# Kernel tuning notes

Hardware: AMD Instinct MI355X
Metric: run time of the kernel (lower is better)

Reference implementation:

```python
import jax, jax.numpy as jnp
import numpy as np
from jax.scipy.special import logsumexp

S, L = 32768, 512  # seq_len, label_num


def setup_inputs() -> dict:
    key = jax.random.key(0)
    k1, k2, k3 = jax.random.split(key, 3)
    logit = jax.random.normal(k1, (S, L), dtype=jnp.float32)   # emissions [S, L]
    labels = jax.random.randint(k2, (S,), 0, L)                # gold path [S]
    T = jax.random.normal(k3, (L, L), dtype=jnp.float32)       # T[next, prev]
    return {"logit": logit, "labels": labels, "T": T}


def _crf_loss(logit, T, labels):
    # Forward algorithm: alpha_t[j] = logsumexp_i(alpha_{t-1}[i] + T[j, i]) + feat_t[j]
    alpha0 = logit[0]

    def step(alpha, feat):
        new_alpha = logsumexp(alpha[None, :] + T, axis=1) + feat  # [L]
        return new_alpha, None

    alpha_final, _ = jax.lax.scan(step, alpha0, logit[1:])
    log_Z = logsumexp(alpha_final)

    # Gold path score: feat_0[y0] + sum_{t>0} (feat_t[y_t] + T[y_t, y_{t-1}])
    emit = logit[0, labels[0]] + jnp.sum(logit[jnp.arange(1, logit.shape[0]), labels[1:]])
    trans = jnp.sum(T[labels[1:], labels[:-1]])
    gold = emit + trans
    return log_Z - gold


def reference(logit, labels, T):
    return _crf_loss(logit, T, labels)
```

## Files before the change

### kernel.cpp

```cpp
#include <hip/hip_runtime.h>
#include <stdint.h>


#define S_LEN 32768
#define L 512
#define CH 16
#define NCF 2048
#define NB  256
#define TPB 1024
#define LN448 6.104793232f
#define LN2   0.6931471806f

#define OFF_EAF  0
#define OFF_EAB  (256*1024)
#define OFF_G    (512*1024)
#define OFF_H    (OFF_G + 2048*512*2)
#define OFF_LSE  (OFF_H + 2048*512*2)
#define OFF_GOLD (OFF_LSE + 4104*4)

#define PL_OFF   0
#define SP_OFF   16384
#define LF_OFF   18432
#define SMEM_TOTAL (18432 + 3*32768)

typedef float v4f __attribute__((ext_vector_type(4)));

__device__ __forceinline__ float b2f(unsigned short u){
  return __uint_as_float(((unsigned)u) << 16);
}
__device__ __forceinline__ unsigned short f2b(float x){
  unsigned u = __float_as_uint(x);
  return (unsigned short)((u + 0x7fffu + ((u >> 16) & 1u)) >> 16);
}
__device__ __forceinline__ unsigned char to_fp8(float v){
  int u = __builtin_amdgcn_cvt_pk_fp8_f32(v, v, 0, false);
  return (unsigned char)(u & 0xff);
}

__device__ __forceinline__ void gl2lds16(const void* g, void* l){
  __builtin_amdgcn_global_load_lds(
      (const __attribute__((address_space(1))) void*)g,
      (__attribute__((address_space(3))) void*)l, 16, 0, 0);
}

__device__ __forceinline__ void lds_sync(){
  asm volatile("s_waitcnt lgkmcnt(0)" ::: "memory");
  __builtin_amdgcn_sched_barrier(0);
  __builtin_amdgcn_s_barrier();
  __builtin_amdgcn_sched_barrier(0);
}
__device__ __forceinline__ void step_sync(){
  asm volatile("s_waitcnt vmcnt(2) lgkmcnt(0)" ::: "memory");
  __builtin_amdgcn_sched_barrier(0);
  __builtin_amdgcn_s_barrier();
  __builtin_amdgcn_sched_barrier(0);
}

__device__ __forceinline__ float waveMax(float v){
  #pragma unroll
  for (int off = 32; off >= 1; off >>= 1) v = fmaxf(v, __shfl_xor(v, off));
  return v;
}
__device__ __forceinline__ float waveSum(float v){
  #pragma unroll
  for (int off = 32; off >= 1; off >>= 1) v += __shfl_xor(v, off);
  return v;
}

__device__ __forceinline__ float blockSum16(float v, float* sred){
  #pragma unroll
  for (int off = 32; off >= 1; off >>= 1) v += __shfl_xor(v, off);
  int wid = threadIdx.x >> 6, lane = threadIdx.x & 63;
  if (lane == 0) sred[wid] = v;
  __syncthreads();
  if (threadIdx.x < 16) {
    float t = sred[threadIdx.x];
    t += __shfl_xor(t, 8); t += __shfl_xor(t, 4);
    t += __shfl_xor(t, 2); t += __shfl_xor(t, 1);
    if (threadIdx.x == 0) sred[16] = t;
  }
  __syncthreads();
  float r = sred[16];
  __syncthreads();
  return r;
}
__device__ __forceinline__ float blockSum8(float v, float* sred){
  #pragma unroll
  for (int off = 32; off >= 1; off >>= 1) v += __shfl_xor(v, off);
  int wid = threadIdx.x >> 6, lane = threadIdx.x & 63;
  if (lane == 0) sred[wid] = v;
  __syncthreads();
  if (threadIdx.x < 8) {
    float t = sred[threadIdx.x];
    t += __shfl_xor(t, 4); t += __shfl_xor(t, 2); t += __shfl_xor(t, 1);
    if (threadIdx.x == 0) sred[8] = t;
  }
  __syncthreads();
  float r = sred[8];
  __syncthreads();
  return r;
}

extern "C" __global__ __launch_bounds__(TPB)
void crf_prep(const float* __restrict__ logit,
              const int* __restrict__ labels,
              const float* __restrict__ T,
              unsigned char* __restrict__ EAf,
              unsigned char* __restrict__ EAb,
              float* __restrict__ part){
  __shared__ float sredG[17];
  const int tidx = threadIdx.x;
  {
    int tid = blockIdx.x*TPB + tidx;
    int r    = tid & 7;
    int lane = (tid >> 3) & 63;
    int kt   = (tid >> 9) & 15;
    int R16  = tid >> 13;
    int j = R16*16 + (lane & 15);
    int i = kt*32 + ((lane >> 4) << 3) + r;
    EAf[tid] = to_fp8(2.0f * __expf(T[j*L + i]));
    EAb[tid] = to_fp8(2.0f * __expf(T[i*L + j]));
  }
  {
    float acc = 0.f;
    if (tidx < 128) {
      int t = blockIdx.x*128 + tidx;
      int yt = labels[t];
      float v = logit[(size_t)t*L + yt];
      if (t > 0) v += T[yt*L + labels[t-1]];
      acc = v;
    }
    float s = blockSum16(acc, sredG);
    if (tidx == 0) part[blockIdx.x] = s;
  }
}

extern "C" __global__ __launch_bounds__(TPB, 4)
void crf_chunks(const float* __restrict__ logit,
                const unsigned char* __restrict__ EAf,
                const unsigned char* __restrict__ EAb,
                unsigned short* __restrict__ G,
                unsigned short* __restrict__ H){
  extern __shared__ __align__(16) char smem[];
  unsigned char* Pl  = (unsigned char*)(smem + PL_OFF);
  float (*sPart)[20] = (float(*)[20])(smem + SP_OFF);
  char*  LF          = smem + LF_OFF;

  const int tidx = threadIdx.x;
  const int w    = tidx >> 6;
  const int lane = tidx & 63;
  const int quad = lane >> 4;
  const int cl   = lane & 15;
  const bool fwd = (blockIdx.x < NB/2);
  const int  b   = fwd ? blockIdx.x : (blockIdx.x - NB/2);
  const int  cg  = fwd ? (b*16 + cl) : (1 + b*16 + cl);
  const int  cgc = min(cg, NCF-1);
  const bool isc0 = fwd && (cg == 0);
  const int  jrow0 = w*32 + quad*4;

  const int  cgw  = fwd ? (b*16 + w) : (1 + b*16 + w);
  const int  cgcw = min(cgw, NCF-1);
  const unsigned swzw = (unsigned)((w & 7) << 4);
  const unsigned so   = ((unsigned)(lane*16)) ^ swzw;

  const long* EAp = (const long*)(fwd ? EAf : EAb);
  long eA[2][16];
  #pragma unroll
  for (int mt = 0; mt < 2; ++mt)
    #pragma unroll
    for (int kt = 0; kt < 16; ++kt)
      eA[mt][kt] = EAp[(((w*2 + mt)*16) + kt)*64 + lane];

  int pladdr0, pladdr1;
  {
    int r0 = jrow0;
    pladdr0 = (r0 >> 5)*512 + ((((r0 >> 3) & 3)*16 + cl) << 3) + (r0 & 7);
    r0 = jrow0 + 16;
    pladdr1 = (r0 >> 5)*512 + ((((r0 >> 3) & 3)*16 + cl) << 3) + (r0 & 7);
  }
  const int bbbase = lane*8;
  const int scl = (cl & 7) << 4;
  const int ib  = w*128 + quad*16;
  const int fa0 = cl*2048 + (ib ^ scl);
  const int fa1 = cl*2048 + ((ib + 64) ^ scl);

  {
    size_t t0 = (size_t)(fwd ? (cgcw*CH + 0) : (cgcw*CH + CH - 2 - 0));
    size_t t1 = (size_t)(fwd ? (cgcw*CH + 1) : (cgcw*CH + CH - 2 - 1));
    const char* r0p = (const char*)logit + t0*(L*4);
    const char* r1p = (const char*)logit + t1*(L*4);
    char* d0 = LF + 0*32768 + w*2048;
    char* d1 = LF + 1*32768 + w*2048;
    gl2lds16(r0p + so, d0);  gl2lds16(r0p + 1024 + so, d0 + 1024);
    gl2lds16(r1p + so, d1);  gl2lds16(r1p + 1024 + so, d1 + 1024);
  }

  v4f v0, v1;
  if (fwd) {
    v0 = (v4f){1.f,1.f,1.f,1.f}; v1 = v0;
  } else {
    const float* ip = logit + (size_t)(cgc*CH + CH - 1)*L + jrow0;
    float4 x0 = *(const float4*)ip, x1 = *(const float4*)(ip + 16);
    v0 = (v4f){__expf(x0.x),__expf(x0.y),__expf(x0.z),__expf(x0.w)};
    v1 = (v4f){__expf(x1.x),__expf(x1.y),__expf(x1.z),__expf(x1.w)};
  }
  float m = 0.0f;
  int par = 0;
  int bo0 = 0, bo1 = 32768, bo2 = 2*32768;

  {
    float mx = fmaxf(fmaxf(fmaxf(v0[0],v0[1]),fmaxf(v0[2],v0[3])),
                     fmaxf(fmaxf(v1[0],v1[1]),fmaxf(v1[2],v1[3])));
    mx = fmaxf(mx, __shfl_xor(mx, 16));
    mx = fmaxf(mx, __shfl_xor(mx, 32));
    if (quad == 0) sPart[cl][w] = mx;
    lds_sync();
    const float4* sp4 = (const float4*)&sPart[cl][0];
    float4 q0 = sp4[0], q1 = sp4[1], q2 = sp4[2], q3 = sp4[3];
    float M = fmaxf(fmaxf(fmaxf(fmaxf(q0.x,q0.y),fmaxf(q0.z,q0.w)),
                          fmaxf(fmaxf(q1.x,q1.y),fmaxf(q1.z,q1.w))),
                    fmaxf(fmaxf(fmaxf(q2.x,q2.y),fmaxf(q2.z,q2.w)),
                          fmaxf(fmaxf(q3.x,q3.y),fmaxf(q3.z,q3.w))));
    float sc = 448.0f / M;
    int u0 = __builtin_amdgcn_cvt_pk_fp8_f32(v0[0]*sc, v0[1]*sc, 0, false);
    u0     = __builtin_amdgcn_cvt_pk_fp8_f32(v0[2]*sc, v0[3]*sc, u0, true);
    *(int*)&Pl[pladdr0] = u0;
    int u1 = __builtin_amdgcn_cvt_pk_fp8_f32(v1[0]*sc, v1[1]*sc, 0, false);
    u1     = __builtin_amdgcn_cvt_pk_fp8_f32(v1[2]*sc, v1[3]*sc, u1, true);
    *(int*)&Pl[pladdr1] = u1;
    m = __logf(M) - LN448;
    step_sync();
  }

  for (int k = 0; k < CH; ++k) {
    const bool last = (k == CH-1);
    const bool useF = fwd || !last;

    {
      const int ks = k + 2;
      const bool ok = fwd ? (ks <= CH-1) : (ks <= CH-2);
      if (ok) {
        size_t t = (size_t)(fwd ? (cgcw*CH + ks) : (cgcw*CH + CH - 2 - ks));
        const char* row = (const char*)logit + t*(L*4);
        char* dst = LF + bo2 + w*2048;
        gl2lds16(row + so, dst);
        gl2lds16(row + 1024 + so, dst + 1024);
      }
    }

    v4f a0 = (v4f){0.f,0.f,0.f,0.f};
    v4f a1 = (v4f){0.f,0.f,0.f,0.f};
    {
      const unsigned char* plr = Pl + par*8192 + bbbase;
      #pragma unroll
      for (int kt = 0; kt < 16; ++kt) {
        long bb = *(const long*)(plr + kt*512);
        a0 = __builtin_amdgcn_mfma_f32_16x16x32_fp8_fp8(eA[0][kt], bb, a0, 0, 0, 0);
        a1 = __builtin_amdgcn_mfma_f32_16x16x32_fp8_fp8(eA[1][kt], bb, a1, 0, 0, 0);
      }
    }

    if (useF) {
      const char* fb = LF + bo0;
      float4 q0 = *(const float4*)(fb + fa0);
      float4 q1 = *(const float4*)(fb + fa1);
      float f0=__expf(q0.x), f1=__expf(q0.y), f2=__expf(q0.z), f3=__expf(q0.w);
      float g0=__expf(q1.x), g1=__expf(q1.y), g2=__expf(q1.z), g3=__expf(q1.w);
      a0 = (v4f){a0[0]*f0, a0[1]*f1, a0[2]*f2, a0[3]*f3};
      a1 = (v4f){a1[0]*g0, a1[1]*g1, a1[2]*g2, a1[3]*g3};
      if (k == 0 && isc0) {
        a0 = (v4f){f0,f1,f2,f3}; a1 = (v4f){g0,g1,g2,g3}; m = 0.0f;
      }
    }

    if (last) {
      if (cg <= NCF-1) {
        float madj = m - (isc0 ? (float)(CH-1) : (float)CH) * LN2;
        unsigned short* dst = (fwd ? G : H) + (size_t)cg*L + jrow0;
        unsigned long long pv =
             (unsigned long long)f2b(__logf(a0[0]) + madj)
          | ((unsigned long long)f2b(__logf(a0[1]) + madj) << 16)
          | ((unsigned long long)f2b(__logf(a0[2]) + madj) << 32)
          | ((unsigned long long)f2b(__logf(a0[3]) + madj) << 48);
        *(unsigned long long*)dst = pv;
        pv = (unsigned long long)f2b(__logf(a1[0]) + madj)
          | ((unsigned long long)f2b(__logf(a1[1]) + madj) << 16)
          | ((unsigned long long)f2b(__logf(a1[2]) + madj) << 32)
          | ((unsigned long long)f2b(__logf(a1[3]) + madj) << 48);
        *(unsigned long long*)(dst + 16) = pv;
      }
    } else {
      float mx = fmaxf(fmaxf(fmaxf(a0[0],a0[1]),fmaxf(a0[2],a0[3])),
                       fmaxf(fmaxf(a1[0],a1[1]),fmaxf(a1[2],a1[3])));
      mx = fmaxf(mx, __shfl_xor(mx, 16));
      mx = fmaxf(mx, __shfl_xor(mx, 32));
      if (quad == 0) sPart[cl][w] = mx;
      lds_sync();
      const float4* sp4 = (const float4*)&sPart[cl][0];
      float4 q0 = sp4[0], q1 = sp4[1], q2 = sp4[2], q3 = sp4[3];
      float M = fmaxf(fmaxf(fmaxf(fmaxf(q0.x,q0.y),fmaxf(q0.z,q0.w)),
                            fmaxf(fmaxf(q1.x,q1.y),fmaxf(q1.z,q1.w))),
                      fmaxf(fmaxf(fmaxf(q2.x,q2.y),fmaxf(q2.z,q2.w)),
                            fmaxf(fmaxf(q3.x,q3.y),fmaxf(q3.z,q3.w))));
      float sc = 448.0f / M;
      int u0 = __builtin_amdgcn_cvt_pk_fp8_f32(a0[0]*sc, a0[1]*sc, 0, false);
      u0     = __builtin_amdgcn_cvt_pk_fp8_f32(a0[2]*sc, a0[3]*sc, u0, true);
      *(int*)&Pl[(par^1)*8192 + pladdr0] = u0;
      int u1 = __builtin_amdgcn_cvt_pk_fp8_f32(a1[0]*sc, a1[1]*sc, 0, false);
      u1     = __builtin_amdgcn_cvt_pk_fp8_f32(a1[2]*sc, a1[3]*sc, u1, true);
      *(int*)&Pl[(par^1)*8192 + pladdr1] = u1;
      m += __logf(M) - LN448;
      step_sync();
      par ^= 1;
      int tmp = bo0; bo0 = bo1; bo1 = bo2; bo2 = tmp;
    }
  }
}

extern "C" __global__ __launch_bounds__(512)
void crf_lse(const unsigned short* __restrict__ G,
             const unsigned short* __restrict__ H,
             float* __restrict__ lsebuf){
  const int tidx = threadIdx.x;
  const int w    = tidx >> 6;
  const int lane = tidx & 63;
  const int g    = blockIdx.x*8 + w;
  const int j8   = lane*8;
  if (g == 0) {
    const unsigned short* p = G + (size_t)(NCF-1)*L + j8;
    ushort4 a = *(const ushort4*)p, bq = *(const ushort4*)(p + 4);
    float v[8] = { b2f(a.x),b2f(a.y),b2f(a.z),b2f(a.w),
                   b2f(bq.x),b2f(bq.y),b2f(bq.z),b2f(bq.w) };
    float mx = v[0];
    #pragma unroll
    for (int r = 1; r < 8; ++r) mx = fmaxf(mx, v[r]);
    mx = waveMax(mx);
    float s = 0.f;
    #pragma unroll
    for (int r = 0; r < 8; ++r) s += __expf(v[r] - mx);
    s = waveSum(s);
    if (lane == 0) lsebuf[2*NCF] = mx + __logf(s);
  } else {
    const unsigned short* hp = H + (size_t)g*L + j8;
    const unsigned short* gp = G + (size_t)(g-1)*L + j8;
    ushort4 ha = *(const ushort4*)hp, hb = *(const ushort4*)(hp + 4);
    ushort4 ga = *(const ushort4*)gp, gb = *(const ushort4*)(gp + 4);
    float hv[8] = { b2f(ha.x),b2f(ha.y),b2f(ha.z),b2f(ha.w),
                    b2f(hb.x),b2f(hb.y),b2f(hb.z),b2f(hb.w) };
    float gv[8] = { b2f(ga.x),b2f(ga.y),b2f(ga.z),b2f(ga.w),
                    b2f(gb.x),b2f(gb.y),b2f(gb.z),b2f(gb.w) };
    float m1 = -3.0e38f, m2 = -3.0e38f;
    #pragma unroll
    for (int r = 0; r < 8; ++r) {
      float a = hv[r] + gv[r];
      m1 = fmaxf(m1, a); m2 = fmaxf(m2, hv[r]);
    }
    m1 = waveMax(m1); m2 = waveMax(m2);
    float s1 = 0.f, s2 = 0.f;
    #pragma unroll
    for (int r = 0; r < 8; ++r) {
      s1 += __expf(hv[r] + gv[r] - m1);
      s2 += __expf(hv[r] - m2);
    }
    s1 = waveSum(s1); s2 = waveSum(s2);
    if (lane == 0) {
      lsebuf[g]       = m1 + __logf(s1);
      lsebuf[NCF + g] = m2 + __logf(s2);
    }
  }
}

extern "C" __global__ __launch_bounds__(512)
void crf_final(const float* __restrict__ lsebuf,
               const float* __restrict__ part,
               float* __restrict__ out){
  __shared__ float sredG[9];
  const int tidx = threadIdx.x;
  float acc = 0.f;
  #pragma unroll
  for (int c = tidx; c < NCF; c += 512)
    if (c >= 1) acc += lsebuf[c] - lsebuf[NCF + c];
  if (tidx < NB) acc -= part[tidx];
  float s = blockSum8(acc, sredG);
  if (tidx == 0) out[0] = lsebuf[2*NCF] + s;
}

extern "C" void kernel_launch(void* const* d_in, const int* in_sizes, int n_in,
                              void* d_out, int out_size, void* d_ws, size_t ws_size,
                              hipStream_t stream){
  const float* logit = (const float*)d_in[0];
  const int* labels  = (const int*)d_in[1];
  const float* T     = (const float*)d_in[2];
  float* out = (float*)d_out;
  char* ws = (char*)d_ws;
  unsigned char* EAf = (unsigned char*)(ws + OFF_EAF);
  unsigned char* EAb = (unsigned char*)(ws + OFF_EAB);
  unsigned short* G  = (unsigned short*)(ws + OFF_G);
  unsigned short* H  = (unsigned short*)(ws + OFF_H);
  float* lsebuf = (float*)(ws + OFF_LSE);
  float* part   = (float*)(ws + OFF_GOLD);

  static bool attr_set = false;
  if (!attr_set) {
    (void)hipFuncSetAttribute((const void*)crf_chunks,
                        hipFuncAttributeMaxDynamicSharedMemorySize, SMEM_TOTAL);
    attr_set = true;
  }

  crf_prep  <<<NB, TPB, 0, stream>>>(logit, labels, T, EAf, EAb, part);
  crf_chunks<<<NB, TPB, SMEM_TOTAL, stream>>>(logit, EAf, EAb, G, H);
  crf_lse   <<<NB, 512, 0, stream>>>(G, H, lsebuf);
  crf_final <<<1, 512, 0, stream>>>(lsebuf, part, out);
}
```

Measured before the change: 131.9 us.

## Halve chunk length and interleave two chunk tiles per block to hide latency

Chunk length drops from 16 to 8, doubling the number of chunks, and each block now processes two independent tiles of 16 chunks, A and B. The MFMA of one tile is interleaved with the max-reduce and fp8 requantize of the other. This hides the serial per-step reduction and barrier latency behind the other tile's matrix work and halves the sequential depth. In exchange it uses more LDS (four 32KB staging buffers) and doubles the G/H intermediate data and the crf_lse grid, which adds work in the later combine stages.

```diff
diff --git a/kernel.cpp b/kernel.cpp
--- a/kernel.cpp
+++ b/kernel.cpp
@@ -4,8 +4,8 @@
 
 #define S_LEN 32768
 #define L 512
-#define CH 16
-#define NCF 2048
+#define CH 8
+#define NCF 4096
 #define NB  256
 #define TPB 1024
 #define LN448 6.104793232f
@@ -14,14 +14,16 @@
 #define OFF_EAF  0
 #define OFF_EAB  (256*1024)
 #define OFF_G    (512*1024)
-#define OFF_H    (OFF_G + 2048*512*2)
-#define OFF_LSE  (OFF_H + 2048*512*2)
-#define OFF_GOLD (OFF_LSE + 4104*4)
-
-#define PL_OFF   0
-#define SP_OFF   16384
-#define LF_OFF   18432
-#define SMEM_TOTAL (18432 + 3*32768)
+#define OFF_H    (OFF_G + NCF*512*2)
+#define OFF_LSE  (OFF_H + NCF*512*2)
+#define OFF_GOLD (OFF_LSE + (2*NCF+8)*4)
+
+#define PL_A   0
+#define PL_B   8192
+#define SPA    16384
+#define SPB    17664
+#define LF     19456
+#define SMEM_TOTAL (19456 + 4*32768)
 
 typedef float v4f __attribute__((ext_vector_type(4)));
 
@@ -49,8 +51,14 @@
   __builtin_amdgcn_s_barrier();
   __builtin_amdgcn_sched_barrier(0);
 }
-__device__ __forceinline__ void step_sync(){
+__device__ __forceinline__ void sync2(){
   asm volatile("s_waitcnt vmcnt(2) lgkmcnt(0)" ::: "memory");
+  __builtin_amdgcn_sched_barrier(0);
+  __builtin_amdgcn_s_barrier();
+  __builtin_amdgcn_sched_barrier(0);
+}
+__device__ __forceinline__ void sync0(){
+  asm volatile("s_waitcnt vmcnt(0) lgkmcnt(0)" ::: "memory");
   __builtin_amdgcn_sched_barrier(0);
   __builtin_amdgcn_s_barrier();
   __builtin_amdgcn_sched_barrier(0);
@@ -142,9 +150,6 @@
                 unsigned short* __restrict__ G,
                 unsigned short* __restrict__ H){
   extern __shared__ __align__(16) char smem[];
-  unsigned char* Pl  = (unsigned char*)(smem + PL_OFF);
-  float (*sPart)[20] = (float(*)[20])(smem + SP_OFF);
-  char*  LF          = smem + LF_OFF;
 
   const int tidx = threadIdx.x;
   const int w    = tidx >> 6;
@@ -153,15 +158,17 @@
   const int cl   = lane & 15;
   const bool fwd = (blockIdx.x < NB/2);
   const int  b   = fwd ? blockIdx.x : (blockIdx.x - NB/2);
-  const int  cg  = fwd ? (b*16 + cl) : (1 + b*16 + cl);
-  const int  cgc = min(cg, NCF-1);
-  const bool isc0 = fwd && (cg == 0);
+  const int  base = (fwd ? 0 : 1) + b*32;
+  const int  cgA  = base + cl;
+  const int  cgB  = cgA + 16;
+  const int  cgcA = min(cgA, NCF-1);
+  const int  cgcB = min(cgB, NCF-1);
+  const bool isc0 = fwd && (cgA == 0);
   const int  jrow0 = w*32 + quad*4;
 
-  const int  cgw  = fwd ? (b*16 + w) : (1 + b*16 + w);
-  const int  cgcw = min(cgw, NCF-1);
-  const unsigned swzw = (unsigned)((w & 7) << 4);
-  const unsigned so   = ((unsigned)(lane*16)) ^ swzw;
+  const int  cgsA = min(base + w,      NCF-1);
+  const int  cgsB = min(base + 16 + w, NCF-1);
+  const unsigned so = ((unsigned)(lane*16)) ^ ((unsigned)((w & 7) << 4));
 
   const long* EAp = (const long*)(fwd ? EAf : EAb);
   long eA[2][16];
@@ -171,148 +178,145 @@
     for (int kt = 0; kt < 16; ++kt)
       eA[mt][kt] = EAp[(((w*2 + mt)*16) + kt)*64 + lane];
 
-  int pladdr0, pladdr1;
-  {
-    int r0 = jrow0;
-    pladdr0 = (r0 >> 5)*512 + ((((r0 >> 3) & 3)*16 + cl) << 3) + (r0 & 7);
-    r0 = jrow0 + 16;
-    pladdr1 = (r0 >> 5)*512 + ((((r0 >> 3) & 3)*16 + cl) << 3) + (r0 & 7);
-  }
-  const int bbbase = lane*8;
+  const int pladdr = (jrow0 >> 5)*512 + ((((jrow0 >> 3) & 3)*16 + cl) << 3)
+                   + (jrow0 & 7);
+  const int bbb = lane*8;
   const int scl = (cl & 7) << 4;
   const int ib  = w*128 + quad*16;
-  const int fa0 = cl*2048 + (ib ^ scl);
-  const int fa1 = cl*2048 + ((ib + 64) ^ scl);
-
-  {
-    size_t t0 = (size_t)(fwd ? (cgcw*CH + 0) : (cgcw*CH + CH - 2 - 0));
-    size_t t1 = (size_t)(fwd ? (cgcw*CH + 1) : (cgcw*CH + CH - 2 - 1));
-    const char* r0p = (const char*)logit + t0*(L*4);
-    const char* r1p = (const char*)logit + t1*(L*4);
-    char* d0 = LF + 0*32768 + w*2048;
-    char* d1 = LF + 1*32768 + w*2048;
-    gl2lds16(r0p + so, d0);  gl2lds16(r0p + 1024 + so, d0 + 1024);
-    gl2lds16(r1p + so, d1);  gl2lds16(r1p + 1024 + so, d1 + 1024);
-  }
-
-  v4f v0, v1;
-  if (fwd) {
-    v0 = (v4f){1.f,1.f,1.f,1.f}; v1 = v0;
-  } else {
-    const float* ip = logit + (size_t)(cgc*CH + CH - 1)*L + jrow0;
-    float4 x0 = *(const float4*)ip, x1 = *(const float4*)(ip + 16);
-    v0 = (v4f){__expf(x0.x),__expf(x0.y),__expf(x0.z),__expf(x0.w)};
-    v1 = (v4f){__expf(x1.x),__expf(x1.y),__expf(x1.z),__expf(x1.w)};
-  }
-  float m = 0.0f;
-  int par = 0;
-  int bo0 = 0, bo1 = 32768, bo2 = 2*32768;
-
-  {
-    float mx = fmaxf(fmaxf(fmaxf(v0[0],v0[1]),fmaxf(v0[2],v0[3])),
-                     fmaxf(fmaxf(v1[0],v1[1]),fmaxf(v1[2],v1[3])));
+  const int fa0 = LF + cl*2048 + (ib ^ scl);
+  const int fa1 = LF + cl*2048 + ((ib + 64) ^ scl);
+
+  auto stage = [&](int tile, int ks){
+    int cgs = tile ? cgsB : cgsA;
+    int t = fwd ? (cgs*CH + ks) : (cgs*CH + CH - 2 - ks);
+    const char* row = (const char*)logit + (size_t)t*(L*4);
+    char* dst = smem + (LF + ((ks & 1) << 16) + (tile << 15) + w*2048);
+    gl2lds16(row + so, dst);
+    gl2lds16(row + 1024 + so, dst + 1024);
+  };
+  auto wmax = [&](v4f x0, v4f x1, int spoff){
+    float mx = fmaxf(fmaxf(fmaxf(x0[0],x0[1]),fmaxf(x0[2],x0[3])),
+                     fmaxf(fmaxf(x1[0],x1[1]),fmaxf(x1[2],x1[3])));
     mx = fmaxf(mx, __shfl_xor(mx, 16));
     mx = fmaxf(mx, __shfl_xor(mx, 32));
-    if (quad == 0) sPart[cl][w] = mx;
-    lds_sync();
-    const float4* sp4 = (const float4*)&sPart[cl][0];
-    float4 q0 = sp4[0], q1 = sp4[1], q2 = sp4[2], q3 = sp4[3];
+    if (quad == 0) *(float*)(smem + spoff + cl*80 + w*4) = mx;
+  };
+  auto s2 = [&](v4f x0, v4f x1, int spoff, int ploff, float& m){
+    const char* spb = smem + spoff + cl*80;
+    float4 q0 = *(const float4*)spb;
+    float4 q1 = *(const float4*)(spb + 16);
+    float4 q2 = *(const float4*)(spb + 32);
+    float4 q3 = *(const float4*)(spb + 48);
     float M = fmaxf(fmaxf(fmaxf(fmaxf(q0.x,q0.y),fmaxf(q0.z,q0.w)),
                           fmaxf(fmaxf(q1.x,q1.y),fmaxf(q1.z,q1.w))),
                     fmaxf(fmaxf(fmaxf(q2.x,q2.y),fmaxf(q2.z,q2.w)),
                           fmaxf(fmaxf(q3.x,q3.y),fmaxf(q3.z,q3.w))));
     float sc = 448.0f / M;
-    int u0 = __builtin_amdgcn_cvt_pk_fp8_f32(v0[0]*sc, v0[1]*sc, 0, false);
-    u0     = __builtin_amdgcn_cvt_pk_fp8_f32(v0[2]*sc, v0[3]*sc, u0, true);
-    *(int*)&Pl[pladdr0] = u0;
-    int u1 = __builtin_amdgcn_cvt_pk_fp8_f32(v1[0]*sc, v1[1]*sc, 0, false);
-    u1     = __builtin_amdgcn_cvt_pk_fp8_f32(v1[2]*sc, v1[3]*sc, u1, true);
-    *(int*)&Pl[pladdr1] = u1;
-    m = __logf(M) - LN448;
-    step_sync();
-  }
-
+    int u0 = __builtin_amdgcn_cvt_pk_fp8_f32(x0[0]*sc, x0[1]*sc, 0, false);
+    u0     = __builtin_amdgcn_cvt_pk_fp8_f32(x0[2]*sc, x0[3]*sc, u0, true);
+    *(int*)(smem + ploff + pladdr) = u0;
+    int u1 = __builtin_amdgcn_cvt_pk_fp8_f32(x1[0]*sc, x1[1]*sc, 0, false);
+    u1     = __builtin_amdgcn_cvt_pk_fp8_f32(x1[2]*sc, x1[3]*sc, u1, true);
+    *(int*)(smem + ploff + pladdr + 256) = u1;
+    m += __logf(M) - LN448;
+  };
+  auto fmul = [&](v4f& x0, v4f& x1, int fbase, bool anchor){
+    const char* fb = smem + fbase;
+    float4 q0 = *(const float4*)(fb + fa0);
+    float4 q1 = *(const float4*)(fb + fa1);
+    float f0=__expf(q0.x), f1=__expf(q0.y), f2=__expf(q0.z), f3=__expf(q0.w);
+    float g0=__expf(q1.x), g1=__expf(q1.y), g2=__expf(q1.z), g3=__expf(q1.w);
+    if (anchor) {
+      x0 = (v4f){f0,f1,f2,f3};  x1 = (v4f){g0,g1,g2,g3};
+    } else {
+      x0 = (v4f){x0[0]*f0, x0[1]*f1, x0[2]*f2, x0[3]*f3};
+      x1 = (v4f){x1[0]*g0, x1[1]*g1, x1[2]*g2, x1[3]*g3};
+    }
+  };
+  auto store_out = [&](v4f x0, v4f x1, float m, int cg, bool anchor){
+    if (cg <= NCF-1) {
+      float madj = m - (anchor ? (float)(CH-1) : (float)CH)*LN2;
+      unsigned short* dst = (fwd ? G : H) + (size_t)cg*L + jrow0;
+      unsigned long long pv =
+           (unsigned long long)f2b(__logf(x0[0]) + madj)
+        | ((unsigned long long)f2b(__logf(x0[1]) + madj) << 16)
+        | ((unsigned long long)f2b(__logf(x0[2]) + madj) << 32)
+        | ((unsigned long long)f2b(__logf(x0[3]) + madj) << 48);
+      *(unsigned long long*)dst = pv;
+      pv = (unsigned long long)f2b(__logf(x1[0]) + madj)
+        | ((unsigned long long)f2b(__logf(x1[1]) + madj) << 16)
+        | ((unsigned long long)f2b(__logf(x1[2]) + madj) << 32)
+        | ((unsigned long long)f2b(__logf(x1[3]) + madj) << 48);
+      *(unsigned long long*)(dst + 16) = pv;
+    }
+  };
+
+  stage(0, 0);  stage(1, 0);
+
+  v4f vA0, vA1, vB0, vB1;
+  if (fwd) {
+    vA0 = (v4f){1.f,1.f,1.f,1.f}; vA1 = vA0; vB0 = vA0; vB1 = vA0;
+  } else {
+    const float* ip = logit + (size_t)(cgcA*CH + CH - 1)*L + jrow0;
+    float4 x0 = *(const float4*)ip, x1 = *(const float4*)(ip + 16);
+    vA0 = (v4f){__expf(x0.x),__expf(x0.y),__expf(x0.z),__expf(x0.w)};
+    vA1 = (v4f){__expf(x1.x),__expf(x1.y),__expf(x1.z),__expf(x1.w)};
+    ip = logit + (size_t)(cgcB*CH + CH - 1)*L + jrow0;
+    x0 = *(const float4*)ip; x1 = *(const float4*)(ip + 16);
+    vB0 = (v4f){__expf(x0.x),__expf(x0.y),__expf(x0.z),__expf(x0.w)};
+    vB1 = (v4f){__expf(x1.x),__expf(x1.y),__expf(x1.z),__expf(x1.w)};
+  }
+  float mA = 0.0f, mB = 0.0f;
+
+  wmax(vA0, vA1, SPA);
+  wmax(vB0, vB1, SPB);
+  lds_sync();
+  s2(vA0, vA1, SPA, PL_A, mA);
+  sync2();
+
+  #pragma unroll
   for (int k = 0; k < CH; ++k) {
     const bool last = (k == CH-1);
-    const bool useF = fwd || !last;
-
     {
-      const int ks = k + 2;
-      const bool ok = fwd ? (ks <= CH-1) : (ks <= CH-2);
-      if (ok) {
-        size_t t = (size_t)(fwd ? (cgcw*CH + ks) : (cgcw*CH + CH - 2 - ks));
-        const char* row = (const char*)logit + t*(L*4);
-        char* dst = LF + bo2 + w*2048;
-        gl2lds16(row + so, dst);
-        gl2lds16(row + 1024 + so, dst + 1024);
-      }
-    }
-
-    v4f a0 = (v4f){0.f,0.f,0.f,0.f};
-    v4f a1 = (v4f){0.f,0.f,0.f,0.f};
-    {
-      const unsigned char* plr = Pl + par*8192 + bbbase;
+      if (fwd ? (k+1 <= CH-1) : (k+1 <= CH-2)) stage(0, k+1);
+      v4f a0 = (v4f){0.f,0.f,0.f,0.f};
+      v4f a1 = (v4f){0.f,0.f,0.f,0.f};
       #pragma unroll
       for (int kt = 0; kt < 16; ++kt) {
-        long bb = *(const long*)(plr + kt*512);
-        a0 = __builtin_amdgcn_mfma_f32_16x16x32_fp8_fp8(eA[0][kt], bb, a0, 0, 0, 0);
-        a1 = __builtin_amdgcn_mfma_f32_16x16x32_fp8_fp8(eA[1][kt], bb, a1, 0, 0, 0);
+        long bbv = *(const long*)(smem + PL_A + bbb + kt*512);
+        a0 = __builtin_amdgcn_mfma_f32_16x16x32_fp8_fp8(eA[0][kt], bbv, a0, 0, 0, 0);
+        a1 = __builtin_amdgcn_mfma_f32_16x16x32_fp8_fp8(eA[1][kt], bbv, a1, 0, 0, 0);
       }
-    }
-
-    if (useF) {
-      const char* fb = LF + bo0;
-      float4 q0 = *(const float4*)(fb + fa0);
-      float4 q1 = *(const float4*)(fb + fa1);
-      float f0=__expf(q0.x), f1=__expf(q0.y), f2=__expf(q0.z), f3=__expf(q0.w);
-      float g0=__expf(q1.x), g1=__expf(q1.y), g2=__expf(q1.z), g3=__expf(q1.w);
-      a0 = (v4f){a0[0]*f0, a0[1]*f1, a0[2]*f2, a0[3]*f3};
-      a1 = (v4f){a1[0]*g0, a1[1]*g1, a1[2]*g2, a1[3]*g3};
-      if (k == 0 && isc0) {
-        a0 = (v4f){f0,f1,f2,f3}; a1 = (v4f){g0,g1,g2,g3}; m = 0.0f;
+      s2(vB0, vB1, SPB, PL_B, mB);
+      if (fwd || !last) fmul(a0, a1, ((k & 1) << 16), k == 0 && isc0);
+      if (k == 0 && isc0) mA = 0.0f;
+      if (last) {
+        store_out(a0, a1, mA, cgA, isc0);
+      } else {
+        vA0 = a0; vA1 = a1;
+        wmax(vA0, vA1, SPA);
       }
-    }
-
-    if (last) {
-      if (cg <= NCF-1) {
-        float madj = m - (isc0 ? (float)(CH-1) : (float)CH) * LN2;
-        unsigned short* dst = (fwd ? G : H) + (size_t)cg*L + jrow0;
-        unsigned long long pv =
-             (unsigned long long)f2b(__logf(a0[0]) + madj)
-          | ((unsigned long long)f2b(__logf(a0[1]) + madj) << 16)
-          | ((unsigned long long)f2b(__logf(a0[2]) + madj) << 32)
-          | ((unsigned long long)f2b(__logf(a0[3]) + madj) << 48);
-        *(unsigned long long*)dst = pv;
-        pv = (unsigned long long)f2b(__logf(a1[0]) + madj)
-          | ((unsigned long long)f2b(__logf(a1[1]) + madj) << 16)
-          | ((unsigned long long)f2b(__logf(a1[2]) + madj) << 32)
-          | ((unsigned long long)f2b(__logf(a1[3]) + madj) << 48);
-        *(unsigned long long*)(dst + 16) = pv;
+      if (k >= CH-2) sync0(); else sync2();
+    }
+    {
+      if (fwd ? (k+1 <= CH-1) : (k+1 <= CH-2)) stage(1, k+1);
+      v4f b0 = (v4f){0.f,0.f,0.f,0.f};
+      v4f b1 = (v4f){0.f,0.f,0.f,0.f};
+      #pragma unroll
+      for (int kt = 0; kt < 16; ++kt) {
+        long bbv = *(const long*)(smem + PL_B + bbb + kt*512);
+        b0 = __builtin_amdgcn_mfma_f32_16x16x32_fp8_fp8(eA[0][kt], bbv, b0, 0, 0, 0);
+        b1 = __builtin_amdgcn_mfma_f32_16x16x32_fp8_fp8(eA[1][kt], bbv, b1, 0, 0, 0);
       }
-    } else {
-      float mx = fmaxf(fmaxf(fmaxf(a0[0],a0[1]),fmaxf(a0[2],a0[3])),
-                       fmaxf(fmaxf(a1[0],a1[1]),fmaxf(a1[2],a1[3])));
-      mx = fmaxf(mx, __shfl_xor(mx, 16));
-      mx = fmaxf(mx, __shfl_xor(mx, 32));
-      if (quad == 0) sPart[cl][w] = mx;
-      lds_sync();
-      const float4* sp4 = (const float4*)&sPart[cl][0];
-      float4 q0 = sp4[0], q1 = sp4[1], q2 = sp4[2], q3 = sp4[3];
-      float M = fmaxf(fmaxf(fmaxf(fmaxf(q0.x,q0.y),fmaxf(q0.z,q0.w)),
-                            fmaxf(fmaxf(q1.x,q1.y),fmaxf(q1.z,q1.w))),
-                      fmaxf(fmaxf(fmaxf(q2.x,q2.y),fmaxf(q2.z,q2.w)),
-                            fmaxf(fmaxf(q3.x,q3.y),fmaxf(q3.z,q3.w))));
-      float sc = 448.0f / M;
-      int u0 = __builtin_amdgcn_cvt_pk_fp8_f32(a0[0]*sc, a0[1]*sc, 0, false);
-      u0     = __builtin_amdgcn_cvt_pk_fp8_f32(a0[2]*sc, a0[3]*sc, u0, true);
-      *(int*)&Pl[(par^1)*8192 + pladdr0] = u0;
-      int u1 = __builtin_amdgcn_cvt_pk_fp8_f32(a1[0]*sc, a1[1]*sc, 0, false);
-      u1     = __builtin_amdgcn_cvt_pk_fp8_f32(a1[2]*sc, a1[3]*sc, u1, true);
-      *(int*)&Pl[(par^1)*8192 + pladdr1] = u1;
-      m += __logf(M) - LN448;
-      step_sync();
-      par ^= 1;
-      int tmp = bo0; bo0 = bo1; bo1 = bo2; bo2 = tmp;
+      if (!last) s2(vA0, vA1, SPA, PL_A, mA);
+      if (fwd || !last) fmul(b0, b1, ((k & 1) << 16) + 32768, false);
+      if (last) {
+        store_out(b0, b1, mB, cgB, false);
+      } else {
+        vB0 = b0; vB1 = b1;
+        wmax(vB0, vB1, SPB);
+        sync2();
+      }
     }
   }
 }
@@ -377,7 +381,6 @@
   __shared__ float sredG[9];
   const int tidx = threadIdx.x;
   float acc = 0.f;
-  #pragma unroll
   for (int c = tidx; c < NCF; c += 512)
     if (c >= 1) acc += lsebuf[c] - lsebuf[NCF + c];
   if (tidx < NB) acc -= part[tidx];
@@ -409,6 +412,6 @@
 
   crf_prep  <<<NB, TPB, 0, stream>>>(logit, labels, T, EAf, EAb, part);
   crf_chunks<<<NB, TPB, SMEM_TOTAL, stream>>>(logit, EAf, EAb, G, H);
-  crf_lse   <<<NB, 512, 0, stream>>>(G, H, lsebuf);
+  crf_lse   <<<NCF/8, 512, 0, stream>>>(G, H, lsebuf);
   crf_final <<<1, 512, 0, stream>>>(lsebuf, part, out);
 }
```

Measured after the change: 136.9 us. +3.8%, slower.
